# Kernel tuning notes

Hardware: AMD Instinct MI355X
Metric: run time of the kernel (lower is better)

The kernel has to match this reference:

```python
import jax, jax.numpy as jnp
import numpy as np


def setup_inputs() -> dict:
    key = jax.random.key(0)
    k1, k2 = jax.random.split(key)
    B, C, N = 2, 3, 16384
    in_pc = jax.random.normal(k1, (B, C, N), dtype=jnp.float32)
    target_pc = jax.random.normal(k2, (B, C, N), dtype=jnp.float32)
    return {"in_pc": in_pc, "target_pc": target_pc}


def reference(in_pc, target_pc):
    # [B,3,N] -> [B,N,3]
    pc1 = jnp.transpose(in_pc, (0, 2, 1))
    pc2 = jnp.transpose(target_pc, (0, 2, 1))
    sqr = (-2.0 * jnp.einsum('bnc,bmc->bnm', pc1, pc2)
           + jnp.sum(pc1 ** 2, -1)[:, :, None]
           + jnp.sum(pc2 ** 2, -1)[:, None, :])
    dist1 = jnp.min(sqr, axis=-1)  # [B,N] NN from pc1 to pc2
    dist2 = jnp.min(sqr, axis=1)   # [B,M] NN from pc2 to pc1
    m_dist = (dist1 + dist2) / 2.0  # requires N == M (as in original)
    return jnp.mean(m_dist)
```

## Files before the change

### kernel.cpp

```cpp
#include <hip/hip_runtime.h>

#define BLK 512
#define MT 32
#define IA 2
#define IB 512
#define TJQ 512
#define SJ 4

typedef __attribute__((ext_vector_type(8))) short short8;
typedef __attribute__((ext_vector_type(16))) float f32x16;

__device__ __forceinline__ unsigned int fmap(float f) {
  unsigned int b = __float_as_uint(f);
  return (b & 0x80000000u) ? ~b : (b | 0x80000000u);
}
__device__ __forceinline__ float funmap(unsigned int u) {
  return __uint_as_float((u & 0x80000000u) ? (u ^ 0x80000000u) : ~u);
}
__device__ __forceinline__ unsigned short f2bf(float f) {
  unsigned int u = __float_as_uint(f);
  u += 0x7FFFu + ((u >> 16) & 1u);
  return (unsigned short)(u >> 16);
}
__device__ __forceinline__ float bf2f(unsigned short h) {
  return __uint_as_float(((unsigned int)h) << 16);
}
__device__ __forceinline__ unsigned int pk(unsigned short a, unsigned short b) {
  return (unsigned int)a | ((unsigned int)b << 16);
}

union FragU { uint4 u; short8 s; };

#define MFMA2(d0, d1, a, b0, b1, c)                                    \
  asm("v_mfma_f32_32x32x16_bf16 %0, %2, %3, %5\n\t"                    \
      "v_mfma_f32_32x32x16_bf16 %1, %2, %4, %5\n\t"                    \
      "s_nop 7\n\t"                                                    \
      "s_nop 7\n\t"                                                    \
      "s_nop 1"                                                        \
      : "=&v"(d0), "=&v"(d1)                                           \
      : "v"(a), "v"(b0), "v"(b1), "v"(c))

#define MIN3(acc, x, y)                                                \
  asm("v_min3_f32 %0, %0, %1, %2" : "+v"(acc) : "v"(x), "v"(y))

__global__ __launch_bounds__(BLK, 4) void cl_mfma(
    const float* __restrict__ A, const float* __restrict__ Bp,
    unsigned int* __restrict__ umin, int N, int jslice, int Bn) {
  __shared__ uint4 sA[2][IB];
  __shared__ uint4 sB[2][TJQ];
  __shared__ float sNP[IB];

  const int zi = blockIdx.z;
  const int dir = zi / Bn;
  const int b = zi - dir * Bn;
  const float* __restrict__ P = dir ? Bp : A;
  const float* __restrict__ Q = dir ? A : Bp;
  unsigned int* __restrict__ um = umin + ((size_t)dir * Bn + b) * N;

  const int t = threadIdx.x;
  const int ib0 = blockIdx.x * IB;
  const int jbase = blockIdx.y * jslice;
  const size_t boff = (size_t)b * 3 * N;
  const unsigned short one = 0x3F80u;

  {
    int i = ib0 + t;
    float x = P[boff + i], y = P[boff + N + i], zz = P[boff + 2 * N + i];
    float ax = -2.f * x, ay = -2.f * y, az = -2.f * zz;
    unsigned short hx = f2bf(ax), hy = f2bf(ay), hz = f2bf(az);
    unsigned short lx = f2bf(ax - bf2f(hx)), ly = f2bf(ay - bf2f(hy)),
                   lz = f2bf(az - bf2f(hz));
    sA[0][t] = make_uint4(pk(hx, hy), pk(hz, lx), pk(ly, lz), pk(hx, hy));
    sA[1][t] = make_uint4(pk(hz, lx), pk(ly, lz), pk(one, one), pk(one, 0));
    sNP[t] = fmaf(zz, zz, fmaf(y, y, x * x));
  }
  __syncthreads();

  const int w = t >> 6, l = t & 63, m = l & 31, g = l >> 5;
  FragU a0u, a1u;
  a0u.u = sA[g][w * (MT * IA) + m];
  a1u.u = sA[g][w * (MT * IA) + MT + m];
  const short8 af0 = a0u.s, af1 = a1u.s;

  float run0[16], run1[16];
  f32x16 zc;
#pragma unroll
  for (int r = 0; r < 16; ++r) { run0[r] = 3.0e38f; run1[r] = 3.0e38f; zc[r] = 0.0f; }

  const int nch = jslice / TJQ;
  float qx = Q[boff + jbase + t];
  float qy = Q[boff + N + jbase + t];
  float qz = Q[boff + 2 * N + jbase + t];

  for (int ch = 0; ch < nch; ++ch) {
    unsigned short hx = f2bf(qx), hy = f2bf(qy), hz = f2bf(qz);
    unsigned short lx = f2bf(qx - bf2f(hx)), ly = f2bf(qy - bf2f(hy)),
                   lz = f2bf(qz - bf2f(hz));
    float nq = fmaf(qz, qz, fmaf(qy, qy, qx * qx));
    unsigned short nh = f2bf(nq);
    float r1 = nq - bf2f(nh);
    unsigned short nm = f2bf(r1);
    unsigned short nl = f2bf(r1 - bf2f(nm));
    uint4 b0s = make_uint4(pk(hx, hy), pk(hz, hx), pk(hy, hz), pk(lx, ly));
    uint4 b1s = make_uint4(pk(lz, lx), pk(ly, lz), pk(nh, nm), pk(nl, 0));

    __syncthreads();
    sB[0][t] = b0s;
    sB[1][t] = b1s;
    {
      int jn = (ch + 1 < nch) ? (jbase + (ch + 1) * TJQ + t) : (jbase + t);
      qx = Q[boff + jn];
      qy = Q[boff + N + jn];
      qz = Q[boff + 2 * N + jn];
    }
    __syncthreads();

#pragma unroll
    for (int jt = 0; jt < TJQ / MT; jt += 2) {
      FragU ba, bb;
      ba.u = sB[g][(jt + 0) * MT + m];
      bb.u = sB[g][(jt + 1) * MT + m];
      f32x16 d0, d1;
      MFMA2(d0, d1, af0, ba.s, bb.s, zc);
#pragma unroll
      for (int r = 0; r < 16; ++r) MIN3(run0[r], d0[r], d1[r]);
      f32x16 d2, d3;
      MFMA2(d2, d3, af1, ba.s, bb.s, zc);
#pragma unroll
      for (int r = 0; r < 16; ++r) MIN3(run1[r], d2[r], d3[r]);
    }
  }

#pragma unroll
  for (int r = 0; r < 16; ++r) {
    float v0 = run0[r], v1 = run1[r];
#pragma unroll
    for (int sh = 1; sh <= 16; sh <<= 1) {
      v0 = fminf(v0, __shfl_xor(v0, sh));
      v1 = fminf(v1, __shfl_xor(v1, sh));
    }
    if (m == 0) {
      int row = (r & 3) + 8 * (r >> 2) + 4 * g;
      int il0 = w * (MT * IA) + row;
      int il1 = il0 + MT;
      atomicMin(&um[ib0 + il0], fmap(v0 + sNP[il0]));
      atomicMin(&um[ib0 + il1], fmap(v1 + sNP[il1]));
    }
  }
}

__global__ __launch_bounds__(256) void cl_reduce(
    const unsigned int* __restrict__ u, float* __restrict__ out, int total) {
  const int t = threadIdx.x;
  const uint4* __restrict__ u4 = (const uint4*)u;
  const int n4 = total / 4;
  const int gid = blockIdx.x * 256 + t;
  const int gstride = gridDim.x * 256;
  double s = 0.0;
  for (int i = gid; i < n4; i += gstride) {
    uint4 v = u4[i];
    s += (double)funmap(v.x) + (double)funmap(v.y) +
         (double)funmap(v.z) + (double)funmap(v.w);
  }
  for (int off = 32; off > 0; off >>= 1) s += __shfl_down(s, off, 64);
  __shared__ double sw[4];
  if ((t & 63) == 0) sw[t >> 6] = s;
  __syncthreads();
  if (t == 0) {
    double tot = sw[0] + sw[1] + sw[2] + sw[3];
    atomicAdd(out, (float)(tot / (double)total));
  }
}

extern "C" void kernel_launch(void* const* d_in, const int* in_sizes, int n_in,
                              void* d_out, int out_size, void* d_ws, size_t ws_size,
                              hipStream_t stream) {
  const float* in_pc = (const float*)d_in[0];
  const float* tgt_pc = (const float*)d_in[1];
  const int B = 2, N = 16384;
  unsigned int* u = (unsigned int*)d_ws;
  float* out = (float*)d_out;

  hipMemsetAsync(u, 0xFF, (size_t)2 * B * N * sizeof(unsigned int), stream);
  hipMemsetAsync(out, 0, sizeof(float), stream);

  const int jslice = N / SJ;
  dim3 grid(N / IB, SJ, 2 * B);
  cl_mfma<<<grid, dim3(BLK), 0, stream>>>(in_pc, tgt_pc, u, N, jslice, B);

  const int total = 2 * B * N;
  cl_reduce<<<dim3(16), dim3(256), 0, stream>>>(u, out, total);
}
```

Measured before the change: 98.50 us.

## Compute both NN directions from one distance tile with column-min via shared atomics

Rather than running two passes (pc1→pc2 and pc2→pc1), each block now computes the full squared distance (with |p|^2 folded into the MFMA via the A/B fragment padding) and reduces both row mins in registers and column mins via shared-memory atomicMin, then flushes column mins to global. This halves the MFMA work and the grid z dimension, while SJ is doubled to keep block count, and launch bounds are relaxed to 2 blocks/CU. It adds per-tile shared atomics and in-register column reductions, and changes the precision split of the norm terms (two bf16 parts instead of three for |q|^2).

```diff
diff --git a/kernel.cpp b/kernel.cpp
--- a/kernel.cpp
+++ b/kernel.cpp
@@ -5,7 +5,7 @@
 #define IA 2
 #define IB 512
 #define TJQ 512
-#define SJ 4
+#define SJ 8
 
 typedef __attribute__((ext_vector_type(8))) short short8;
 typedef __attribute__((ext_vector_type(16))) float f32x16;
@@ -31,31 +31,32 @@
 
 union FragU { uint4 u; short8 s; };
 
-#define MFMA2(d0, d1, a, b0, b1, c)                                    \
-  asm("v_mfma_f32_32x32x16_bf16 %0, %2, %3, %5\n\t"                    \
-      "v_mfma_f32_32x32x16_bf16 %1, %2, %4, %5\n\t"                    \
-      "s_nop 7\n\t"                                                    \
-      "s_nop 7\n\t"                                                    \
-      "s_nop 1"                                                        \
-      : "=&v"(d0), "=&v"(d1)                                           \
-      : "v"(a), "v"(b0), "v"(b1), "v"(c))
-
-#define MIN3(acc, x, y)                                                \
+#define MFMA4(d0, d1, d2, d3, a0, a1, b0, b1, c)                        \
+  asm("v_mfma_f32_32x32x16_bf16 %0, %4, %6, %8\n\t"                     \
+      "v_mfma_f32_32x32x16_bf16 %1, %4, %7, %8\n\t"                     \
+      "v_mfma_f32_32x32x16_bf16 %2, %5, %6, %8\n\t"                     \
+      "v_mfma_f32_32x32x16_bf16 %3, %5, %7, %8\n\t"                     \
+      "s_nop 7\n\t"                                                     \
+      "s_nop 7\n\t"                                                     \
+      "s_nop 1"                                                         \
+      : "=&v"(d0), "=&v"(d1), "=&v"(d2), "=&v"(d3)                      \
+      : "v"(a0), "v"(a1), "v"(b0), "v"(b1), "v"(c))
+
+#define MIN3(acc, x, y)                                                 \
   asm("v_min3_f32 %0, %0, %1, %2" : "+v"(acc) : "v"(x), "v"(y))
 
-__global__ __launch_bounds__(BLK, 4) void cl_mfma(
+__global__ __launch_bounds__(BLK, 2) void cl_mfma(
     const float* __restrict__ A, const float* __restrict__ Bp,
     unsigned int* __restrict__ umin, int N, int jslice, int Bn) {
   __shared__ uint4 sA[2][IB];
   __shared__ uint4 sB[2][TJQ];
-  __shared__ float sNP[IB];
-
-  const int zi = blockIdx.z;
-  const int dir = zi / Bn;
-  const int b = zi - dir * Bn;
-  const float* __restrict__ P = dir ? Bp : A;
-  const float* __restrict__ Q = dir ? A : Bp;
-  unsigned int* __restrict__ um = umin + ((size_t)dir * Bn + b) * N;
+  __shared__ unsigned int scmin[2048];
+
+  const int b = blockIdx.z;
+  const float* __restrict__ P = A;
+  const float* __restrict__ Q = Bp;
+  unsigned int* __restrict__ u1 = umin + (size_t)b * N;
+  unsigned int* __restrict__ u2 = umin + ((size_t)Bn + b) * N;
 
   const int t = threadIdx.x;
   const int ib0 = blockIdx.x * IB;
@@ -63,6 +64,8 @@
   const size_t boff = (size_t)b * 3 * N;
   const unsigned short one = 0x3F80u;
 
+#pragma unroll
+  for (int c = 0; c < 4; ++c) scmin[c * BLK + t] = 0xFFFFFFFFu;
   {
     int i = ib0 + t;
     float x = P[boff + i], y = P[boff + N + i], zz = P[boff + 2 * N + i];
@@ -70,9 +73,11 @@
     unsigned short hx = f2bf(ax), hy = f2bf(ay), hz = f2bf(az);
     unsigned short lx = f2bf(ax - bf2f(hx)), ly = f2bf(ay - bf2f(hy)),
                    lz = f2bf(az - bf2f(hz));
+    float np = fmaf(zz, zz, fmaf(y, y, x * x));
+    unsigned short nph = f2bf(np);
+    unsigned short npl = f2bf(np - bf2f(nph));
     sA[0][t] = make_uint4(pk(hx, hy), pk(hz, lx), pk(ly, lz), pk(hx, hy));
-    sA[1][t] = make_uint4(pk(hz, lx), pk(ly, lz), pk(one, one), pk(one, 0));
-    sNP[t] = fmaf(zz, zz, fmaf(y, y, x * x));
+    sA[1][t] = make_uint4(pk(hz, lx), pk(ly, lz), pk(one, one), pk(nph, npl));
   }
   __syncthreads();
 
@@ -97,12 +102,10 @@
     unsigned short lx = f2bf(qx - bf2f(hx)), ly = f2bf(qy - bf2f(hy)),
                    lz = f2bf(qz - bf2f(hz));
     float nq = fmaf(qz, qz, fmaf(qy, qy, qx * qx));
-    unsigned short nh = f2bf(nq);
-    float r1 = nq - bf2f(nh);
-    unsigned short nm = f2bf(r1);
-    unsigned short nl = f2bf(r1 - bf2f(nm));
+    unsigned short nqh = f2bf(nq);
+    unsigned short nqm = f2bf(nq - bf2f(nqh));
     uint4 b0s = make_uint4(pk(hx, hy), pk(hz, hx), pk(hy, hz), pk(lx, ly));
-    uint4 b1s = make_uint4(pk(lz, lx), pk(ly, lz), pk(nh, nm), pk(nl, 0));
+    uint4 b1s = make_uint4(pk(lz, lx), pk(ly, lz), pk(nqh, nqm), pk(one, one));
 
     __syncthreads();
     sB[0][t] = b0s;
@@ -120,14 +123,21 @@
       FragU ba, bb;
       ba.u = sB[g][(jt + 0) * MT + m];
       bb.u = sB[g][(jt + 1) * MT + m];
-      f32x16 d0, d1;
-      MFMA2(d0, d1, af0, ba.s, bb.s, zc);
+      f32x16 d0, d1, d2, d3;
+      MFMA4(d0, d1, d2, d3, af0, af1, ba.s, bb.s, zc);
 #pragma unroll
       for (int r = 0; r < 16; ++r) MIN3(run0[r], d0[r], d1[r]);
-      f32x16 d2, d3;
-      MFMA2(d2, d3, af1, ba.s, bb.s, zc);
 #pragma unroll
       for (int r = 0; r < 16; ++r) MIN3(run1[r], d2[r], d3[r]);
+      float ca = fminf(d0[0], d2[0]);
+      float cb = fminf(d1[0], d3[0]);
+#pragma unroll
+      for (int r = 1; r < 16; ++r) {
+        ca = fminf(ca, fminf(d0[r], d2[r]));
+        cb = fminf(cb, fminf(d1[r], d3[r]));
+      }
+      atomicMin(&scmin[ch * TJQ + (jt + 0) * MT + m], fmap(ca));
+      atomicMin(&scmin[ch * TJQ + (jt + 1) * MT + m], fmap(cb));
     }
   }
 
@@ -143,9 +153,16 @@
       int row = (r & 3) + 8 * (r >> 2) + 4 * g;
       int il0 = w * (MT * IA) + row;
       int il1 = il0 + MT;
-      atomicMin(&um[ib0 + il0], fmap(v0 + sNP[il0]));
-      atomicMin(&um[ib0 + il1], fmap(v1 + sNP[il1]));
-    }
+      atomicMin(&u1[ib0 + il0], fmap(v0));
+      atomicMin(&u1[ib0 + il1], fmap(v1));
+    }
+  }
+
+  __syncthreads();
+#pragma unroll
+  for (int c = 0; c < 4; ++c) {
+    int col = c * BLK + t;
+    atomicMin(&u2[jbase + col], scmin[col]);
   }
 }
 
@@ -185,7 +202,7 @@
   hipMemsetAsync(out, 0, sizeof(float), stream);
 
   const int jslice = N / SJ;
-  dim3 grid(N / IB, SJ, 2 * B);
+  dim3 grid(N / IB, SJ, B);
   cl_mfma<<<grid, dim3(BLK), 0, stream>>>(in_pc, tgt_pc, u, N, jslice, B);
 
   const int total = 2 * B * N;
```

Measured after the change: 116.3 us. 1.18x slower.
